# Optimization experiments

Hardware: AMD Instinct MI355X
Metric: run time of the kernel (lower is better)

## Reference

```python
import jax, jax.numpy as jnp
import numpy as np

T, B, DIN, DLAT = 512, 64, 256, 512

def setup_inputs() -> dict:
    key = jax.random.key(0)
    ks = jax.random.split(key, 5)
    return {
        "x": jax.random.normal(ks[0], (T, B, DIN), dtype=jnp.float32),
        "h0": jax.random.normal(ks[1], (B, DLAT), dtype=jnp.float32),
        "W_in": jax.random.normal(ks[2], (DLAT, DIN), dtype=jnp.float32) * (1.0 / np.sqrt(DIN)),
        "W_h": jax.random.normal(ks[3], (DLAT, DLAT), dtype=jnp.float32) * (1.0 / np.sqrt(DLAT)),
        "b_h": jax.random.normal(ks[4], (DLAT,), dtype=jnp.float32) * 0.01,
    }

def reference(x, h0, W_in, W_h, b_h):
    # x: [T, B, dim_in]; h0: [B, dim_latent]
    # one_step: relu(x @ W_in^T + h @ W_h^T + b_h); stack hidden states over time
    def step(h, x_t):
        h_new = jax.nn.relu(x_t @ W_in.T + h @ W_h.T + b_h)
        return h_new, h_new
    _, h_seq = jax.lax.scan(step, h0, x)  # h_seq: [T, B, dim_latent]
    return h_seq
```

## Files before the change

kernel.cpp:

```cpp
#include <hip/hip_runtime.h>

#define TSTEPS 512
#define BATCH  64
#define DIN    256
#define DLAT   512

typedef _Float16 half8_t __attribute__((ext_vector_type(8)));
typedef float    f32x4  __attribute__((ext_vector_type(4)));

#define WS_WF_OFF  (512u * 1024u)
#define WS_TIER2   (512u * 1024u)
#define WS_TIER1   (768u * 1024u)

__device__ __forceinline__ void barrier_lds_only()
{
    __builtin_amdgcn_sched_barrier(0);
    asm volatile("s_waitcnt lgkmcnt(0)\n\ts_barrier" ::: "memory");
    __builtin_amdgcn_sched_barrier(0);
}

#define BM 64
#define BN 64
#define BK 32

__global__ __launch_bounds__(256)
void precompute_gemm(const float* __restrict__ x,
                     const float* __restrict__ Win,
                     const float* __restrict__ bh,
                     float* __restrict__ P)
{
    __shared__ float As[BM][BK + 1];
    __shared__ float Ws[BN][BK + 1];
    const int m0  = blockIdx.y * BM;
    const int n0  = blockIdx.x * BN;
    const int tid = threadIdx.x;
    const int tx  = tid & 15;
    const int ty  = tid >> 4;
    const int lr  = tid >> 2;
    const int lc  = (tid & 3) * 8;

    float acc[4][4] = {};

    for (int kk = 0; kk < DIN; kk += BK) {
        const float* ax = x   + (size_t)(m0 + lr) * DIN + kk + lc;
        const float* aw = Win + (size_t)(n0 + lr) * DIN + kk + lc;
        float4 a0 = *(const float4*)(ax);
        float4 a1 = *(const float4*)(ax + 4);
        float4 w0 = *(const float4*)(aw);
        float4 w1 = *(const float4*)(aw + 4);
        As[lr][lc+0]=a0.x; As[lr][lc+1]=a0.y; As[lr][lc+2]=a0.z; As[lr][lc+3]=a0.w;
        As[lr][lc+4]=a1.x; As[lr][lc+5]=a1.y; As[lr][lc+6]=a1.z; As[lr][lc+7]=a1.w;
        Ws[lr][lc+0]=w0.x; Ws[lr][lc+1]=w0.y; Ws[lr][lc+2]=w0.z; Ws[lr][lc+3]=w0.w;
        Ws[lr][lc+4]=w1.x; Ws[lr][lc+5]=w1.y; Ws[lr][lc+6]=w1.z; Ws[lr][lc+7]=w1.w;
        __syncthreads();
        #pragma unroll
        for (int k = 0; k < BK; ++k) {
            float a[4], w[4];
            #pragma unroll
            for (int i = 0; i < 4; ++i) a[i] = As[ty*4+i][k];
            #pragma unroll
            for (int j = 0; j < 4; ++j) w[j] = Ws[tx*4+j][k];
            #pragma unroll
            for (int i = 0; i < 4; ++i)
                #pragma unroll
                for (int j = 0; j < 4; ++j)
                    acc[i][j] += a[i] * w[j];
        }
        __syncthreads();
    }

    float4 bv = *(const float4*)(bh + n0 + tx*4);
    #pragma unroll
    for (int i = 0; i < 4; ++i) {
        float4 v;
        v.x = acc[i][0] + bv.x; v.y = acc[i][1] + bv.y;
        v.z = acc[i][2] + bv.z; v.w = acc[i][3] + bv.w;
        *(float4*)(P + (size_t)(m0 + ty*4 + i) * DLAT + n0 + tx*4) = v;
    }
}

__global__ __launch_bounds__(256)
void pack_wh_mfma(const float* __restrict__ Wh, _Float16* __restrict__ Wm)
{
    const int idx  = blockIdx.x * 256 + threadIdx.x;
    const int lane = idx & 63;
    const int tile = idx >> 6;
    const int kt   = tile >> 5;
    const int ntg  = tile & 31;
    const int n    = ntg * 16 + (lane & 15);
    const int k0   = kt * 32 + (lane >> 4) * 8;
    half8_t v;
    #pragma unroll
    for (int e = 0; e < 8; ++e)
        v[e] = (_Float16)Wh[(size_t)n * DLAT + k0 + e];
    *(half8_t*)(Wm + (size_t)idx * 8) = v;
}

__global__ __launch_bounds__(256)
void pack_win_f16(const float* __restrict__ Win, _Float16* __restrict__ Wf)
{
    const int idx  = blockIdx.x * 256 + threadIdx.x;
    const int lane = idx & 63;
    const int tile = idx >> 6;
    const int kt   = tile >> 5;
    const int ntg  = tile & 31;
    const int n    = ntg * 16 + (lane & 15);
    const int k0   = kt * 32 + (lane >> 4) * 8;
    half8_t v;
    #pragma unroll
    for (int e = 0; e < 8; ++e)
        v[e] = (_Float16)Win[(size_t)n * DIN + k0 + e];
    *(half8_t*)(Wf + (size_t)idx * 8) = v;
}

__global__ __launch_bounds__(256)
void precompute_mfma(const float* __restrict__ x,
                     const half8_t* __restrict__ Wf,
                     const float* __restrict__ bh,
                     float* __restrict__ P)
{
    const int tid  = threadIdx.x;
    const int wave = tid >> 6, lane = tid & 63;
    const int wm   = wave >> 1, wn = wave & 1;
    const int m0   = (blockIdx.x >> 2) * 128 + wm * 64;
    const int n0   = (blockIdx.x & 3) * 128 + wn * 64;
    const int col  = lane & 15, rg = lane >> 4;

    float bv[4];
    #pragma unroll
    for (int nt = 0; nt < 4; ++nt) bv[nt] = bh[n0 + nt * 16 + col];

    f32x4 C[4][4] = {};

    #pragma unroll
    for (int kt = 0; kt < 8; ++kt) {
        half8_t A[4];
        #pragma unroll
        for (int mt = 0; mt < 4; ++mt) {
            const float* xp = x + (size_t)(m0 + mt * 16 + col) * DIN
                                + kt * 32 + rg * 8;
            float4 a = *(const float4*)xp;
            float4 b = *(const float4*)(xp + 4);
            half8_t v;
            v[0] = (_Float16)a.x; v[1] = (_Float16)a.y;
            v[2] = (_Float16)a.z; v[3] = (_Float16)a.w;
            v[4] = (_Float16)b.x; v[5] = (_Float16)b.y;
            v[6] = (_Float16)b.z; v[7] = (_Float16)b.w;
            A[mt] = v;
        }
        half8_t B[4];
        #pragma unroll
        for (int nt = 0; nt < 4; ++nt)
            B[nt] = Wf[(size_t)((kt * 32 + (n0 >> 4) + nt) * 64) + lane];
        #pragma unroll
        for (int mt = 0; mt < 4; ++mt)
            #pragma unroll
            for (int nt = 0; nt < 4; ++nt)
                C[mt][nt] = __builtin_amdgcn_mfma_f32_16x16x32_f16(
                                A[mt], B[nt], C[mt][nt], 0, 0, 0);
    }

    #pragma unroll
    for (int mt = 0; mt < 4; ++mt)
        #pragma unroll
        for (int nt = 0; nt < 4; ++nt) {
            #pragma unroll
            for (int r = 0; r < 4; ++r) {
                const int m = m0 + mt * 16 + rg * 4 + r;
                P[(size_t)m * DLAT + n0 + nt * 16 + col] = C[mt][nt][r] + bv[nt];
            }
        }
}

__global__ __launch_bounds__(512, 2)
void rnn_scan_mfma8(const half8_t* __restrict__ Wm,
                    const float* __restrict__ h0,
                    float* __restrict__ out)
{
    __shared__ half8_t  ldsB[8 * 14 * 64];
    __shared__ _Float16 hbuf[2][DLAT];

    const int b    = blockIdx.x;
    const int tid  = threadIdx.x;
    const int w    = tid >> 6;
    const int lane = tid & 63;

    half8_t bfr[50];
    #pragma unroll
    for (int kt = 0; kt < 16; ++kt)
        #pragma unroll
        for (int nt = 0; nt < 4; ++nt) {
            const int f = kt * 4 + nt;
            half8_t v = Wm[(size_t)((kt * 32 + w * 4 + nt) * 64) + lane];
            if (f < 50) bfr[f] = v;
            else        ldsB[(w * 14 + (f - 50)) * 64 + lane] = v;
        }

    hbuf[0][tid] = (_Float16)h0[(size_t)b * DLAT + tid];
    __syncthreads();

    for (int t = 0; t < TSTEPS; ++t) {
        const int cur = t & 1, nxt = cur ^ 1;
        float* orow = out + ((size_t)t * BATCH + b) * DLAT;

        float pv = orow[w * 64 + lane];

        f32x4 C[4] = {};
        #pragma unroll
        for (int kt = 0; kt < 16; ++kt) {
            half8_t A = *(const half8_t*)&hbuf[cur][kt * 32 + (lane >> 4) * 8];
            #pragma unroll
            for (int nt = 0; nt < 4; ++nt) {
                const int f = kt * 4 + nt;
                half8_t B = (f < 50) ? bfr[f]
                                     : ldsB[(w * 14 + (f - 50)) * 64 + lane];
                C[nt] = __builtin_amdgcn_mfma_f32_16x16x32_f16(A, B, C[nt], 0, 0, 0);
            }
        }

        const int g4 = lane >> 4;
        float m = (g4 == 0) ? C[0][0]
                : (g4 == 1) ? C[1][0]
                : (g4 == 2) ? C[2][0]
                :             C[3][0];
        float v = fmaxf(m + pv, 0.f);
        orow[w * 64 + lane] = v;
        hbuf[nxt][w * 64 + lane] = (_Float16)v;
        barrier_lds_only();
    }
}

__global__ __launch_bounds__(512)
void rnn_scan_row(const float* __restrict__ Wh,
                  const float* __restrict__ h0,
                  float* __restrict__ out)
{
    __shared__ float h[DLAT];
    const int b = blockIdx.x;
    const int r = threadIdx.x;
    h[r] = h0[(size_t)b * DLAT + r];
    __syncthreads();
    const float* wrow = Wh + (size_t)r * DLAT;
    for (int t = 0; t < TSTEPS; ++t) {
        float* orow = out + ((size_t)t * BATCH + b) * DLAT;
        float acc = orow[r];
        #pragma unroll 8
        for (int k = 0; k < DLAT; k += 4) {
            float4 w  = *(const float4*)(wrow + k);
            float4 hv = *(const float4*)&h[k];
            acc += w.x*hv.x + w.y*hv.y + w.z*hv.z + w.w*hv.w;
        }
        float v = fmaxf(acc, 0.f);
        __syncthreads();
        h[r] = v;
        orow[r] = v;
        __syncthreads();
    }
}

extern "C" void kernel_launch(void* const* d_in, const int* in_sizes, int n_in,
                              void* d_out, int out_size, void* d_ws, size_t ws_size,
                              hipStream_t stream)
{
    const float* x    = (const float*)d_in[0];
    const float* h0   = (const float*)d_in[1];
    const float* Win  = (const float*)d_in[2];
    const float* Wh   = (const float*)d_in[3];
    const float* bh   = (const float*)d_in[4];
    float* out = (float*)d_out;

    if (ws_size >= WS_TIER1) {
        _Float16* Wm = (_Float16*)d_ws;
        _Float16* Wf = (_Float16*)((char*)d_ws + WS_WF_OFF);
        pack_wh_mfma<<<128, 256, 0, stream>>>(Wh, Wm);
        pack_win_f16<<<64, 256, 0, stream>>>(Win, Wf);
        precompute_mfma<<<1024, 256, 0, stream>>>(x, (const half8_t*)Wf, bh, out);
        rnn_scan_mfma8<<<BATCH, 512, 0, stream>>>((const half8_t*)Wm, h0, out);
    } else if (ws_size >= WS_TIER2) {
        _Float16* Wm = (_Float16*)d_ws;
        dim3 gA(DLAT / BN, (TSTEPS * BATCH) / BM);
        pack_wh_mfma<<<128, 256, 0, stream>>>(Wh, Wm);
        precompute_gemm<<<gA, 256, 0, stream>>>(x, Win, bh, out);
        rnn_scan_mfma8<<<BATCH, 512, 0, stream>>>((const half8_t*)Wm, h0, out);
    } else {
        dim3 gA(DLAT / BN, (TSTEPS * BATCH) / BM);
        precompute_gemm<<<gA, 256, 0, stream>>>(x, Win, bh, out);
        rnn_scan_row<<<BATCH, 512, 0, stream>>>(Wh, h0, out);
    }
}
```

Measured before the change: 754.9 us.

## Replace per-step workgroup barrier with per-wave LDS flags in RNN scan

The recurrent scan kernel drops the full workgroup barrier at the end of each timestep. Each wave instead publishes a per-wave flag in LDS once it has written its slice of the next hidden state. Consumers process K-chunks in a rotated order starting with a neighbour's chunk, spin-waiting only on the flag of the wave that produced each chunk, so they can start MFMAs before every wave has finished. Register and LDS weight fragments are reordered to match the rotation. The intent is to remove barrier stalls and let waves overlap; the cost is spin-polling with s_sleep and extra atomic LDS loads, and correctness now depends on flag ordering instead of the barrier.

```diff
diff --git a/kernel.cpp b/kernel.cpp
--- a/kernel.cpp
+++ b/kernel.cpp
@@ -11,13 +11,6 @@
 #define WS_WF_OFF  (512u * 1024u)
 #define WS_TIER2   (512u * 1024u)
 #define WS_TIER1   (768u * 1024u)
-
-__device__ __forceinline__ void barrier_lds_only()
-{
-    __builtin_amdgcn_sched_barrier(0);
-    asm volatile("s_waitcnt lgkmcnt(0)\n\ts_barrier" ::: "memory");
-    __builtin_amdgcn_sched_barrier(0);
-}
 
 #define BM 64
 #define BN 64
@@ -173,12 +166,13 @@
 }
 
 __global__ __launch_bounds__(512, 2)
-void rnn_scan_mfma8(const half8_t* __restrict__ Wm,
-                    const float* __restrict__ h0,
-                    float* __restrict__ out)
+void rnn_scan_mfma_pc(const half8_t* __restrict__ Wm,
+                      const float* __restrict__ h0,
+                      float* __restrict__ out)
 {
     __shared__ half8_t  ldsB[8 * 14 * 64];
     __shared__ _Float16 hbuf[2][DLAT];
+    __shared__ int      flags[8];
 
     const int b    = blockIdx.x;
     const int tid  = threadIdx.x;
@@ -187,35 +181,60 @@
 
     half8_t bfr[50];
     #pragma unroll
-    for (int kt = 0; kt < 16; ++kt)
-        #pragma unroll
-        for (int nt = 0; nt < 4; ++nt) {
-            const int f = kt * 4 + nt;
-            half8_t v = Wm[(size_t)((kt * 32 + w * 4 + nt) * 64) + lane];
-            if (f < 50) bfr[f] = v;
-            else        ldsB[(w * 14 + (f - 50)) * 64 + lane] = v;
-        }
+    for (int s = 0; s < 8; ++s) {
+        const int ktp = (w + 1 + s) & 7;
+        #pragma unroll
+        for (int q = 0; q < 2; ++q)
+            #pragma unroll
+            for (int nt = 0; nt < 4; ++nt) {
+                const int j = s * 8 + q * 4 + nt;
+                half8_t v = Wm[(size_t)(((2 * ktp + q) * 32 + w * 4 + nt) * 64)
+                               + lane];
+                if (j < 50) bfr[j] = v;
+                else        ldsB[(w * 14 + (j - 50)) * 64 + lane] = v;
+            }
+    }
 
     hbuf[0][tid] = (_Float16)h0[(size_t)b * DLAT + tid];
+    if (tid < 8) flags[tid] = 0;
     __syncthreads();
 
     for (int t = 0; t < TSTEPS; ++t) {
         const int cur = t & 1, nxt = cur ^ 1;
         float* orow = out + ((size_t)t * BATCH + b) * DLAT;
-
         float pv = orow[w * 64 + lane];
 
         f32x4 C[4] = {};
-        #pragma unroll
-        for (int kt = 0; kt < 16; ++kt) {
-            half8_t A = *(const half8_t*)&hbuf[cur][kt * 32 + (lane >> 4) * 8];
-            #pragma unroll
-            for (int nt = 0; nt < 4; ++nt) {
-                const int f = kt * 4 + nt;
-                half8_t B = (f < 50) ? bfr[f]
-                                     : ldsB[(w * 14 + (f - 50)) * 64 + lane];
-                C[nt] = __builtin_amdgcn_mfma_f32_16x16x32_f16(A, B, C[nt], 0, 0, 0);
+        int fcur = __hip_atomic_load(&flags[(w + 1) & 7], __ATOMIC_ACQUIRE,
+                                     __HIP_MEMORY_SCOPE_WORKGROUP);
+        #pragma unroll
+        for (int s = 0; s < 8; ++s) {
+            const int ktp = (w + 1 + s) & 7;
+            while (fcur < t) {
+                __builtin_amdgcn_s_sleep(1);
+                fcur = __hip_atomic_load(&flags[ktp], __ATOMIC_ACQUIRE,
+                                         __HIP_MEMORY_SCOPE_WORKGROUP);
             }
+            __builtin_amdgcn_sched_barrier(0);
+            int fnext = 0;
+            if (s < 7)
+                fnext = __hip_atomic_load(&flags[(w + 2 + s) & 7],
+                                          __ATOMIC_ACQUIRE,
+                                          __HIP_MEMORY_SCOPE_WORKGROUP);
+            #pragma unroll
+            for (int q = 0; q < 2; ++q) {
+                const int kt = 2 * ktp + q;
+                half8_t A = *(const half8_t*)&hbuf[cur][kt * 32 + (lane >> 4) * 8];
+                #pragma unroll
+                for (int nt = 0; nt < 4; ++nt) {
+                    const int j = s * 8 + q * 4 + nt;
+                    half8_t B = (j < 50) ? bfr[j]
+                                         : ldsB[(w * 14 + (j - 50)) * 64 + lane];
+                    C[nt] = __builtin_amdgcn_mfma_f32_16x16x32_f16(
+                                A, B, C[nt], 0, 0, 0);
+                }
+            }
+            fcur = fnext;
         }
 
         const int g4 = lane >> 4;
@@ -226,7 +245,8 @@
         float v = fmaxf(m + pv, 0.f);
         orow[w * 64 + lane] = v;
         hbuf[nxt][w * 64 + lane] = (_Float16)v;
-        barrier_lds_only();
+        __hip_atomic_store(&flags[w], t + 1, __ATOMIC_RELEASE,
+                           __HIP_MEMORY_SCOPE_WORKGROUP);
     }
 }
 
@@ -275,13 +295,13 @@
         pack_wh_mfma<<<128, 256, 0, stream>>>(Wh, Wm);
         pack_win_f16<<<64, 256, 0, stream>>>(Win, Wf);
         precompute_mfma<<<1024, 256, 0, stream>>>(x, (const half8_t*)Wf, bh, out);
-        rnn_scan_mfma8<<<BATCH, 512, 0, stream>>>((const half8_t*)Wm, h0, out);
+        rnn_scan_mfma_pc<<<BATCH, 512, 0, stream>>>((const half8_t*)Wm, h0, out);
     } else if (ws_size >= WS_TIER2) {
         _Float16* Wm = (_Float16*)d_ws;
         dim3 gA(DLAT / BN, (TSTEPS * BATCH) / BM);
         pack_wh_mfma<<<128, 256, 0, stream>>>(Wh, Wm);
         precompute_gemm<<<gA, 256, 0, stream>>>(x, Win, bh, out);
-        rnn_scan_mfma8<<<BATCH, 512, 0, stream>>>((const half8_t*)Wm, h0, out);
+        rnn_scan_mfma_pc<<<BATCH, 512, 0, stream>>>((const half8_t*)Wm, h0, out);
     } else {
         dim3 gA(DLAT / BN, (TSTEPS * BATCH) / BM);
         precompute_gemm<<<gA, 256, 0, stream>>>(x, Win, bh, out);
```

Measured after the change: 807.0 us. 6.9% more time.

## Stagger K order per wavefront and software-pipeline hidden-state LDS loads

Applied to the files above, without the earlier changes.

Each wavefront in the recurrent scan now starts its K loop at a different offset (2*w), so the eight waves read different hidden-state chunks at the same moment and contend less for LDS. The hidden-state A fragments are double-buffered in registers and prefetched two k-tiles ahead so LDS latency overlaps the MFMAs. Wave priority is raised around the MFMA loop. Register-held weight fragments drop from 50 to 48, with more of them spilled to LDS, which adds some LDS traffic per step.

```diff
diff --git a/kernel.cpp b/kernel.cpp
--- a/kernel.cpp
+++ b/kernel.cpp
@@ -173,28 +173,31 @@
 }
 
 __global__ __launch_bounds__(512, 2)
-void rnn_scan_mfma8(const half8_t* __restrict__ Wm,
-                    const float* __restrict__ h0,
-                    float* __restrict__ out)
-{
-    __shared__ half8_t  ldsB[8 * 14 * 64];
+void rnn_scan_stag(const half8_t* __restrict__ Wm,
+                   const float* __restrict__ h0,
+                   float* __restrict__ out)
+{
+    __shared__ half8_t  ldsB[8 * 16 * 64];
     __shared__ _Float16 hbuf[2][DLAT];
 
     const int b    = blockIdx.x;
     const int tid  = threadIdx.x;
     const int w    = tid >> 6;
     const int lane = tid & 63;
-
-    half8_t bfr[50];
-    #pragma unroll
-    for (int kt = 0; kt < 16; ++kt)
+    const int kt0  = 2 * w;
+
+    half8_t bfr[48];
+    #pragma unroll
+    for (int s = 0; s < 16; ++s) {
+        const int kt = (kt0 + s) & 15;
         #pragma unroll
         for (int nt = 0; nt < 4; ++nt) {
-            const int f = kt * 4 + nt;
+            const int j = s * 4 + nt;
             half8_t v = Wm[(size_t)((kt * 32 + w * 4 + nt) * 64) + lane];
-            if (f < 50) bfr[f] = v;
-            else        ldsB[(w * 14 + (f - 50)) * 64 + lane] = v;
-        }
+            if (j < 48) bfr[j] = v;
+            else        ldsB[(w * 16 + (j - 48)) * 64 + lane] = v;
+        }
+    }
 
     hbuf[0][tid] = (_Float16)h0[(size_t)b * DLAT + tid];
     __syncthreads();
@@ -202,21 +205,44 @@
     for (int t = 0; t < TSTEPS; ++t) {
         const int cur = t & 1, nxt = cur ^ 1;
         float* orow = out + ((size_t)t * BATCH + b) * DLAT;
-
         float pv = orow[w * 64 + lane];
 
         f32x4 C[4] = {};
-        #pragma unroll
-        for (int kt = 0; kt < 16; ++kt) {
-            half8_t A = *(const half8_t*)&hbuf[cur][kt * 32 + (lane >> 4) * 8];
-            #pragma unroll
-            for (int nt = 0; nt < 4; ++nt) {
-                const int f = kt * 4 + nt;
-                half8_t B = (f < 50) ? bfr[f]
-                                     : ldsB[(w * 14 + (f - 50)) * 64 + lane];
-                C[nt] = __builtin_amdgcn_mfma_f32_16x16x32_f16(A, B, C[nt], 0, 0, 0);
+        half8_t Ap[2][2];
+        #pragma unroll
+        for (int i = 0; i < 4; ++i) {
+            const int kt = (kt0 + i) & 15;
+            Ap[i >> 1][i & 1] =
+                *(const half8_t*)&hbuf[cur][kt * 32 + (lane >> 4) * 8];
+        }
+        __builtin_amdgcn_s_setprio(1);
+        #pragma unroll
+        for (int c = 0; c < 8; ++c) {
+            const int pb = c & 1;
+            #pragma unroll
+            for (int i = 0; i < 2; ++i) {
+                const int s = c * 2 + i;
+                half8_t Av = Ap[pb][i];
+                #pragma unroll
+                for (int nt = 0; nt < 4; ++nt) {
+                    const int j = s * 4 + nt;
+                    half8_t B = (j < 48) ? bfr[j]
+                                         : ldsB[(w * 16 + (j - 48)) * 64 + lane];
+                    C[nt] = __builtin_amdgcn_mfma_f32_16x16x32_f16(
+                                Av, B, C[nt], 0, 0, 0);
+                }
             }
-        }
+            if (c < 6) {
+                #pragma unroll
+                for (int i = 0; i < 2; ++i) {
+                    const int s = (c + 2) * 2 + i;
+                    const int kt = (kt0 + s) & 15;
+                    Ap[pb][i] =
+                        *(const half8_t*)&hbuf[cur][kt * 32 + (lane >> 4) * 8];
+                }
+            }
+        }
+        __builtin_amdgcn_s_setprio(0);
 
         const int g4 = lane >> 4;
         float m = (g4 == 0) ? C[0][0]
@@ -275,13 +301,13 @@
         pack_wh_mfma<<<128, 256, 0, stream>>>(Wh, Wm);
         pack_win_f16<<<64, 256, 0, stream>>>(Win, Wf);
         precompute_mfma<<<1024, 256, 0, stream>>>(x, (const half8_t*)Wf, bh, out);
-        rnn_scan_mfma8<<<BATCH, 512, 0, stream>>>((const half8_t*)Wm, h0, out);
+        rnn_scan_stag<<<BATCH, 512, 0, stream>>>((const half8_t*)Wm, h0, out);
     } else if (ws_size >= WS_TIER2) {
         _Float16* Wm = (_Float16*)d_ws;
         dim3 gA(DLAT / BN, (TSTEPS * BATCH) / BM);
         pack_wh_mfma<<<128, 256, 0, stream>>>(Wh, Wm);
         precompute_gemm<<<gA, 256, 0, stream>>>(x, Win, bh, out);
-        rnn_scan_mfma8<<<BATCH, 512, 0, stream>>>((const half8_t*)Wm, h0, out);
+        rnn_scan_stag<<<BATCH, 512, 0, stream>>>((const half8_t*)Wm, h0, out);
     } else {
         dim3 gA(DLAT / BN, (TSTEPS * BATCH) / BM);
         precompute_gemm<<<gA, 256, 0, stream>>>(x, Win, bh, out);
```

Result: faster. 705.1 us (-6.6%).
